# Kernel tuning notes

Measured on AMD Instinct MI355X. Metric: run time of the kernel, lower is better.

Reference implementation:

```python
import jax, jax.numpy as jnp
import numpy as np

B = 1024
NUM_FEATURES = 800  # 10*10 grid * 8 channels
L1, L2, L3, NUM_CLASSES = 1024, 15, 32, 1
STRIDE = 10  # max(1, (96+2*1-3)//(10-1))
VIS_THRESH = 0.0


def setup_inputs() -> dict:
    key = jax.random.key(0)
    ks = jax.random.split(key, 9)
    images = jax.random.normal(ks[0], (B, 3, 96, 96), dtype=jnp.float32)
    conv_w = jax.random.normal(ks[1], (8, 3, 3, 3), dtype=jnp.float32) * 0.1
    ft_w = jax.random.normal(ks[2], (NUM_FEATURES, L1), dtype=jnp.float32) * 0.1
    ft_b = jnp.zeros((L1,), dtype=jnp.float32)
    w1 = jax.random.normal(ks[3], (L2, L1), dtype=jnp.float32) * (1.0 / np.sqrt(L1))
    b1 = jax.random.normal(ks[4], (L2,), dtype=jnp.float32) * 0.01
    w2 = jax.random.normal(ks[5], (L3, L2), dtype=jnp.float32) * (1.0 / np.sqrt(L2))
    b2 = jax.random.normal(ks[6], (L3,), dtype=jnp.float32) * 0.01
    w3 = jax.random.normal(ks[7], (NUM_CLASSES, L3), dtype=jnp.float32) * (1.0 / np.sqrt(L3))
    b3 = jax.random.normal(ks[8], (NUM_CLASSES,), dtype=jnp.float32) * 0.01
    return {"images": images, "conv_w": conv_w, "ft_w": ft_w, "ft_b": ft_b,
            "w1": w1, "b1": b1, "w2": w2, "b2": b2, "w3": w3, "b3": b3}


def reference(images, conv_w, ft_w, ft_b, w1, b1, w2, b2, w3, b3):
    # Conv2d(3->8, k=3, stride=10, pad=1, no bias): [B,3,96,96] -> [B,8,10,10]
    x = jax.lax.conv_general_dilated(
        images, conv_w, window_strides=(STRIDE, STRIDE),
        padding=((1, 1), (1, 1)),
        dimension_numbers=("NCHW", "OIHW", "NCHW"))
    x = jnp.clip(x, -1.0, 1.0)  # Hardtanh
    # training-mode soft binarization
    binary = jax.nn.sigmoid(10.0 * (x - VIS_THRESH))
    bflat = binary.reshape(binary.shape[0], -1)  # [B, 800]
    # _to_sparse_features keeps only entries > 0.5; FeatureTransformer then does
    # a ragged gather-scale-sum == masked dense matmul with the FT weights.
    vals = jnp.where(bflat > 0.5, bflat, 0.0)
    features = vals @ ft_w + ft_b  # [B, L1]
    l0 = jnp.clip(features, 0.0, 1.0)
    h = L1 // 2
    s0, s1 = l0[:, :h], l0[:, h:]
    l0c = jnp.concatenate([s0 * s1, s0], axis=1) * (127.0 / 128.0)  # [B, L1]
    # SimpleClassifier: Linear->ReLU->Linear->ReLU->Linear
    h1 = jax.nn.relu(l0c @ w1.T + b1)
    h2 = jax.nn.relu(h1 @ w2.T + b2)
    out = h2 @ w3.T + b3  # [B, NUM_CLASSES]
    return out
```

## Files before the change

### kernel.cpp

```cpp
#include <hip/hip_runtime.h>

typedef unsigned short u16;
typedef unsigned int   u32;
typedef __attribute__((ext_vector_type(8))) short short8;
typedef __attribute__((ext_vector_type(4))) float f32x4;

__device__ __forceinline__ u16 f2bf(float f) {
    union { float f; u32 i; } v; v.f = f;
    u32 x = v.i;
    return (u16)((x + 0x7fffu + ((x >> 16) & 1u)) >> 16);
}
__device__ __forceinline__ float bf2f(u16 u) {
    union { u32 i; float f; } v; v.i = ((u32)u) << 16; return v.f;
}

__global__ __launch_bounds__(256) void k1_fused(
    const float* __restrict__ images,
    const float* __restrict__ conv_w,
    const float* __restrict__ ft_w,
    u16* __restrict__ vh, u16* __restrict__ vl,
    u16* __restrict__ bth, u16* __restrict__ btl)
{
    __shared__ float img_s[3][29][96];
    __shared__ float w[216];
    __shared__ float tile[32][33];

    int t = threadIdx.x;

    if (blockIdx.x >= 1024) {
        int bid = blockIdx.x - 1024;
        int kb = bid / 32, nb = bid - kb * 32;
        int k0 = kb * 32, n0 = nb * 32;
        int tx = t & 31, ty = t >> 5;
        #pragma unroll
        for (int i = 0; i < 4; i++) {
            int k = ty + i * 8;
            tile[k][tx] = ft_w[(k0 + k) * 1024 + n0 + tx];
        }
        __syncthreads();
        #pragma unroll
        for (int i = 0; i < 4; i++) {
            int n = ty + i * 8;
            float wv = tile[tx][n];
            u16 hi = f2bf(wv);
            float lo = wv - bf2f(hi);
            bth[(n0 + n) * 800 + k0 + tx] = hi;
            btl[(n0 + n) * 800 + k0 + tx] = f2bf(lo);
        }
        return;
    }

    int b = blockIdx.x;
    if (t < 216) w[t] = conv_w[t];

    for (int i = t; i < 3 * 29 * 96; i += 256) {
        int ch  = i / (29 * 96);
        int rem = i - ch * (29 * 96);
        int lr  = rem / 96;
        int x   = rem - lr * 96;
        int ih  = 10 * ((lr + 1) / 3) + (lr + 1) % 3 - 1;
        img_s[ch][lr][x] = images[((b * 3 + ch) * 96 + ih) * 96 + x];
    }
    __syncthreads();

    for (int ridx = t; ridx < 800; ridx += 256) {
        int o  = ridx / 100;
        int p  = ridx - o * 100;
        int oh = p / 10;
        int ow = p - oh * 10;

        float sum = 0.0f;
        #pragma unroll
        for (int ic = 0; ic < 3; ic++) {
            const float* wc = &w[o * 27 + ic * 9];
            #pragma unroll
            for (int kh = 0; kh < 3; kh++) {
                int lr = 3 * oh + kh - 1;
                if (lr < 0) continue;
                #pragma unroll
                for (int kw = 0; kw < 3; kw++) {
                    int iw = ow * 10 + kw - 1;
                    if (iw < 0) continue;
                    sum = fmaf(img_s[ic][lr][iw], wc[kh * 3 + kw], sum);
                }
            }
        }
        float xc = fminf(fmaxf(sum, -1.0f), 1.0f);
        float binary = 1.0f / (1.0f + __expf(-10.0f * xc));
        float v = (binary > 0.5f) ? binary : 0.0f;
        u16 hi = f2bf(v);
        vh[b * 800 + ridx] = hi;
        vl[b * 800 + ridx] = f2bf(v - bf2f(hi));
    }
}

__global__ __launch_bounds__(256) void k2_mfma(
    const u16* __restrict__ Ah, const u16* __restrict__ Al,
    const u16* __restrict__ Bh, const u16* __restrict__ Bl,
    const float* __restrict__ bias,
    float* __restrict__ C)
{
    __shared__ u16 sAh[64 * 40], sAl[64 * 40], sBh[64 * 40], sBl[64 * 40];
    int t = threadIdx.x;
    int m0 = blockIdx.y * 64, n0 = blockIdx.x * 64;
    int w = t >> 6, lane = t & 63;
    int quad = lane >> 4, lo4 = lane & 15;
    int wm = (w >> 1) * 32, wn = (w & 1) * 32;

    int sr = t >> 2;
    int sq = t & 3;
    const u16* gAh = Ah + (m0 + sr) * 800 + sq * 8;
    const u16* gAl = Al + (m0 + sr) * 800 + sq * 8;
    const u16* gBh = Bh + (n0 + sr) * 800 + sq * 8;
    const u16* gBl = Bl + (n0 + sr) * 800 + sq * 8;
    int sdst = sr * 40 + sq * 8;

    f32x4 acc[2][2] = {};

    uint4 rAh = *(const uint4*)(gAh);
    uint4 rAl = *(const uint4*)(gAl);
    uint4 rBh = *(const uint4*)(gBh);
    uint4 rBl = *(const uint4*)(gBl);

    for (int k0 = 0; k0 < 800; k0 += 32) {
        *(uint4*)&sAh[sdst] = rAh;
        *(uint4*)&sAl[sdst] = rAl;
        *(uint4*)&sBh[sdst] = rBh;
        *(uint4*)&sBl[sdst] = rBl;
        __syncthreads();

        if (k0 + 32 < 800) {
            rAh = *(const uint4*)(gAh + k0 + 32);
            rAl = *(const uint4*)(gAl + k0 + 32);
            rBh = *(const uint4*)(gBh + k0 + 32);
            rBl = *(const uint4*)(gBl + k0 + 32);
        }

        short8 a_h[2], a_l[2], b_h[2], b_l[2];
        #pragma unroll
        for (int f = 0; f < 2; f++) {
            int mi = (wm + f * 16 + lo4) * 40 + quad * 8;
            a_h[f] = *(const short8*)&sAh[mi];
            a_l[f] = *(const short8*)&sAl[mi];
            int ni = (wn + f * 16 + lo4) * 40 + quad * 8;
            b_h[f] = *(const short8*)&sBh[ni];
            b_l[f] = *(const short8*)&sBl[ni];
        }
        #pragma unroll
        for (int fm = 0; fm < 2; fm++)
            #pragma unroll
            for (int fn = 0; fn < 2; fn++) {
                acc[fm][fn] = __builtin_amdgcn_mfma_f32_16x16x32_bf16(a_h[fm], b_h[fn], acc[fm][fn], 0, 0, 0);
                acc[fm][fn] = __builtin_amdgcn_mfma_f32_16x16x32_bf16(a_h[fm], b_l[fn], acc[fm][fn], 0, 0, 0);
                acc[fm][fn] = __builtin_amdgcn_mfma_f32_16x16x32_bf16(a_l[fm], b_h[fn], acc[fm][fn], 0, 0, 0);
            }
        __syncthreads();
    }

    #pragma unroll
    for (int fm = 0; fm < 2; fm++) {
        #pragma unroll
        for (int fn = 0; fn < 2; fn++) {
            int n = n0 + wn + fn * 16 + lo4;
            float bv = bias[n];
            #pragma unroll
            for (int r = 0; r < 4; r++) {
                int m = m0 + wm + fm * 16 + quad * 4 + r;
                float v = acc[fm][fn][r] + bv;
                C[m * 1024 + n] = fminf(fmaxf(v, 0.f), 1.f);
            }
        }
    }
}

__global__ __launch_bounds__(256) void k3_tail(
    const float* __restrict__ l0,
    const float* __restrict__ w1,
    const float* __restrict__ b1,
    const float* __restrict__ w2,
    const float* __restrict__ b2,
    const float* __restrict__ w3,
    const float* __restrict__ b3,
    float* __restrict__ out)
{
    int wave = threadIdx.x >> 6;
    int lane = threadIdx.x & 63;
    int b = blockIdx.x * 4 + wave;
    const float* row = l0 + b * 1024;
    const float cc = 0.9921875f;

    float acc[15];
    #pragma unroll
    for (int j = 0; j < 15; j++) acc[j] = 0.f;

    #pragma unroll
    for (int i = 0; i < 2; i++) {
        int k4 = (lane + i * 64) * 4;
        float4 x0 = *(const float4*)(row + k4);
        float4 x1 = *(const float4*)(row + k4 + 512);
        float4 va, vb;
        va.x = x0.x * x1.x * cc; va.y = x0.y * x1.y * cc;
        va.z = x0.z * x1.z * cc; va.w = x0.w * x1.w * cc;
        vb.x = x0.x * cc; vb.y = x0.y * cc;
        vb.z = x0.z * cc; vb.w = x0.w * cc;
        #pragma unroll
        for (int j = 0; j < 15; j++) {
            float4 wa = *(const float4*)(w1 + j * 1024 + k4);
            float4 wb = *(const float4*)(w1 + j * 1024 + k4 + 512);
            acc[j] = fmaf(va.x, wa.x, acc[j]); acc[j] = fmaf(va.y, wa.y, acc[j]);
            acc[j] = fmaf(va.z, wa.z, acc[j]); acc[j] = fmaf(va.w, wa.w, acc[j]);
            acc[j] = fmaf(vb.x, wb.x, acc[j]); acc[j] = fmaf(vb.y, wb.y, acc[j]);
            acc[j] = fmaf(vb.z, wb.z, acc[j]); acc[j] = fmaf(vb.w, wb.w, acc[j]);
        }
    }

    #pragma unroll
    for (int j = 0; j < 15; j++) {
        #pragma unroll
        for (int m = 32; m >= 1; m >>= 1)
            acc[j] += __shfl_xor(acc[j], m, 64);
    }
    float h1[15];
    #pragma unroll
    for (int j = 0; j < 15; j++) h1[j] = fmaxf(acc[j] + b1[j], 0.f);

    float contrib = 0.f;
    if (lane < 32) {
        float h2 = b2[lane];
        #pragma unroll
        for (int j = 0; j < 15; j++) h2 = fmaf(h1[j], w2[lane * 15 + j], h2);
        h2 = fmaxf(h2, 0.f);
        contrib = h2 * w3[lane];
    }
    #pragma unroll
    for (int m = 32; m >= 1; m >>= 1) contrib += __shfl_xor(contrib, m, 64);

    if (lane == 0) out[b] = contrib + b3[0];
}

extern "C" void kernel_launch(void* const* d_in, const int* in_sizes, int n_in,
                              void* d_out, int out_size, void* d_ws, size_t ws_size,
                              hipStream_t stream) {
    const float* images = (const float*)d_in[0];
    const float* conv_w = (const float*)d_in[1];
    const float* ft_w   = (const float*)d_in[2];
    const float* ft_b   = (const float*)d_in[3];
    const float* w1     = (const float*)d_in[4];
    const float* b1     = (const float*)d_in[5];
    const float* w2     = (const float*)d_in[6];
    const float* b2     = (const float*)d_in[7];
    const float* w3     = (const float*)d_in[8];
    const float* b3     = (const float*)d_in[9];
    float* out = (float*)d_out;

    const int NV = 1024 * 800;
    u16* vh  = (u16*)d_ws;
    u16* vl  = vh + NV;
    u16* bth = vl + NV;
    u16* btl = bth + NV;
    float* l0 = (float*)(btl + NV);

    k1_fused<<<1824, 256, 0, stream>>>(images, conv_w, ft_w, vh, vl, bth, btl);
    k2_mfma<<<dim3(16, 16), 256, 0, stream>>>(vh, vl, bth, btl, ft_b, l0);
    k3_tail<<<256, 256, 0, stream>>>(l0, w1, b1, w2, b2, w3, b3, out);
}
```

Before: 209.7 us.

## Merge three kernels into one cooperative persistent kernel with grid syncs

Replaces the three separate launches (conv/weight-convert, MFMA GEMM, MLP tail) with a single cooperative kernel of 256 blocks that loops over the stage-1 jobs, then uses grid-wide syncs between stages. It reuses shared memory through a union across phases. The aim is to remove inter-kernel launch gaps and tail bubbles. In exchange, stage 1 runs with only 256 resident blocks instead of 1824, grid sync itself has a cost, and the old three-kernel path is kept as a fallback if the cooperative launch fails.

```diff
diff --git a/kernel.cpp b/kernel.cpp
--- a/kernel.cpp
+++ b/kernel.cpp
@@ -1,4 +1,7 @@
 #include <hip/hip_runtime.h>
+#include <hip/hip_cooperative_groups.h>
+
+namespace cg = cooperative_groups;
 
 typedef unsigned short u16;
 typedef unsigned int   u32;
@@ -12,6 +15,229 @@
 }
 __device__ __forceinline__ float bf2f(u16 u) {
     union { u32 i; float f; } v; v.i = ((u32)u) << 16; return v.f;
+}
+
+struct P1 { float img[3][29][96]; float w[216]; float tile[32][33]; };
+struct P2 { u16 sAh[64 * 40]; u16 sAl[64 * 40]; u16 sBh[64 * 40]; u16 sBl[64 * 40]; };
+union SMem { P1 p1; P2 p2; };
+
+__global__ __launch_bounds__(256) void k_all(
+    const float* __restrict__ images,
+    const float* __restrict__ conv_w,
+    const float* __restrict__ ft_w,
+    const float* __restrict__ ft_b,
+    const float* __restrict__ w1, const float* __restrict__ b1,
+    const float* __restrict__ w2, const float* __restrict__ b2,
+    const float* __restrict__ w3, const float* __restrict__ b3,
+    float* __restrict__ out,
+    u16* __restrict__ vh, u16* __restrict__ vl,
+    u16* __restrict__ bth, u16* __restrict__ btl,
+    float* __restrict__ l0)
+{
+    __shared__ SMem smem;
+    int t = threadIdx.x;
+
+    for (int job = blockIdx.x; job < 1824; job += 256) {
+        __syncthreads();
+        if (job >= 1024) {
+            int bid = job - 1024;
+            int kb = bid / 32, nb = bid - kb * 32;
+            int k0 = kb * 32, n0 = nb * 32;
+            int tx = t & 31, ty = t >> 5;
+            #pragma unroll
+            for (int i = 0; i < 4; i++) {
+                int k = ty + i * 8;
+                smem.p1.tile[k][tx] = ft_w[(k0 + k) * 1024 + n0 + tx];
+            }
+            __syncthreads();
+            #pragma unroll
+            for (int i = 0; i < 4; i++) {
+                int n = ty + i * 8;
+                float wv = smem.p1.tile[tx][n];
+                u16 hi = f2bf(wv);
+                float lo = wv - bf2f(hi);
+                bth[(n0 + n) * 800 + k0 + tx] = hi;
+                btl[(n0 + n) * 800 + k0 + tx] = f2bf(lo);
+            }
+        } else {
+            int b = job;
+            if (t < 216) smem.p1.w[t] = conv_w[t];
+            for (int i = t; i < 3 * 29 * 96; i += 256) {
+                int ch  = i / (29 * 96);
+                int rem = i - ch * (29 * 96);
+                int lr  = rem / 96;
+                int x   = rem - lr * 96;
+                int ih  = 10 * ((lr + 1) / 3) + (lr + 1) % 3 - 1;
+                smem.p1.img[ch][lr][x] = images[((b * 3 + ch) * 96 + ih) * 96 + x];
+            }
+            __syncthreads();
+
+            for (int ridx = t; ridx < 800; ridx += 256) {
+                int o  = ridx / 100;
+                int p  = ridx - o * 100;
+                int oh = p / 10;
+                int ow = p - oh * 10;
+
+                float sum = 0.0f;
+                #pragma unroll
+                for (int ic = 0; ic < 3; ic++) {
+                    const float* wc = &smem.p1.w[o * 27 + ic * 9];
+                    #pragma unroll
+                    for (int kh = 0; kh < 3; kh++) {
+                        int lr = 3 * oh + kh - 1;
+                        if (lr < 0) continue;
+                        #pragma unroll
+                        for (int kw = 0; kw < 3; kw++) {
+                            int iw = ow * 10 + kw - 1;
+                            if (iw < 0) continue;
+                            sum = fmaf(smem.p1.img[ic][lr][iw], wc[kh * 3 + kw], sum);
+                        }
+                    }
+                }
+                float xc = fminf(fmaxf(sum, -1.0f), 1.0f);
+                float binary = 1.0f / (1.0f + __expf(-10.0f * xc));
+                float v = (binary > 0.5f) ? binary : 0.0f;
+                u16 hi = f2bf(v);
+                vh[b * 800 + ridx] = hi;
+                vl[b * 800 + ridx] = f2bf(v - bf2f(hi));
+            }
+        }
+    }
+
+    cg::this_grid().sync();
+
+    {
+        u16* sAh = smem.p2.sAh; u16* sAl = smem.p2.sAl;
+        u16* sBh = smem.p2.sBh; u16* sBl = smem.p2.sBl;
+
+        int m0 = (blockIdx.x >> 4) * 64, n0 = (blockIdx.x & 15) * 64;
+        int w = t >> 6, lane = t & 63;
+        int quad = lane >> 4, lo4 = lane & 15;
+        int wm = (w >> 1) * 32, wn = (w & 1) * 32;
+
+        int sr = t >> 2;
+        int sq = t & 3;
+        const u16* gAh = vh + (m0 + sr) * 800 + sq * 8;
+        const u16* gAl = vl + (m0 + sr) * 800 + sq * 8;
+        const u16* gBh = bth + (n0 + sr) * 800 + sq * 8;
+        const u16* gBl = btl + (n0 + sr) * 800 + sq * 8;
+        int sdst = sr * 40 + sq * 8;
+
+        f32x4 acc[2][2] = {};
+
+        uint4 rAh = *(const uint4*)(gAh);
+        uint4 rAl = *(const uint4*)(gAl);
+        uint4 rBh = *(const uint4*)(gBh);
+        uint4 rBl = *(const uint4*)(gBl);
+
+        for (int k0 = 0; k0 < 800; k0 += 32) {
+            *(uint4*)&sAh[sdst] = rAh;
+            *(uint4*)&sAl[sdst] = rAl;
+            *(uint4*)&sBh[sdst] = rBh;
+            *(uint4*)&sBl[sdst] = rBl;
+            __syncthreads();
+
+            if (k0 + 32 < 800) {
+                rAh = *(const uint4*)(gAh + k0 + 32);
+                rAl = *(const uint4*)(gAl + k0 + 32);
+                rBh = *(const uint4*)(gBh + k0 + 32);
+                rBl = *(const uint4*)(gBl + k0 + 32);
+            }
+
+            short8 a_h[2], a_l[2], b_h[2], b_l[2];
+            #pragma unroll
+            for (int f = 0; f < 2; f++) {
+                int mi = (wm + f * 16 + lo4) * 40 + quad * 8;
+                a_h[f] = *(const short8*)&sAh[mi];
+                a_l[f] = *(const short8*)&sAl[mi];
+                int ni = (wn + f * 16 + lo4) * 40 + quad * 8;
+                b_h[f] = *(const short8*)&sBh[ni];
+                b_l[f] = *(const short8*)&sBl[ni];
+            }
+            #pragma unroll
+            for (int fm = 0; fm < 2; fm++)
+                #pragma unroll
+                for (int fn = 0; fn < 2; fn++) {
+                    acc[fm][fn] = __builtin_amdgcn_mfma_f32_16x16x32_bf16(a_h[fm], b_h[fn], acc[fm][fn], 0, 0, 0);
+                    acc[fm][fn] = __builtin_amdgcn_mfma_f32_16x16x32_bf16(a_h[fm], b_l[fn], acc[fm][fn], 0, 0, 0);
+                    acc[fm][fn] = __builtin_amdgcn_mfma_f32_16x16x32_bf16(a_l[fm], b_h[fn], acc[fm][fn], 0, 0, 0);
+                }
+            __syncthreads();
+        }
+
+        #pragma unroll
+        for (int fm = 0; fm < 2; fm++) {
+            #pragma unroll
+            for (int fn = 0; fn < 2; fn++) {
+                int n = n0 + wn + fn * 16 + lo4;
+                float bv = ft_b[n];
+                #pragma unroll
+                for (int r = 0; r < 4; r++) {
+                    int m = m0 + wm + fm * 16 + quad * 4 + r;
+                    float v = acc[fm][fn][r] + bv;
+                    l0[m * 1024 + n] = fminf(fmaxf(v, 0.f), 1.f);
+                }
+            }
+        }
+    }
+
+    cg::this_grid().sync();
+
+    {
+        int wave = t >> 6;
+        int lane = t & 63;
+        int b = blockIdx.x * 4 + wave;
+        const float* row = l0 + b * 1024;
+        const float cc = 0.9921875f;
+
+        float acc[15];
+        #pragma unroll
+        for (int j = 0; j < 15; j++) acc[j] = 0.f;
+
+        #pragma unroll
+        for (int i = 0; i < 2; i++) {
+            int k4 = (lane + i * 64) * 4;
+            float4 x0 = *(const float4*)(row + k4);
+            float4 x1 = *(const float4*)(row + k4 + 512);
+            float4 va, vb;
+            va.x = x0.x * x1.x * cc; va.y = x0.y * x1.y * cc;
+            va.z = x0.z * x1.z * cc; va.w = x0.w * x1.w * cc;
+            vb.x = x0.x * cc; vb.y = x0.y * cc;
+            vb.z = x0.z * cc; vb.w = x0.w * cc;
+            #pragma unroll
+            for (int j = 0; j < 15; j++) {
+                float4 wa = *(const float4*)(w1 + j * 1024 + k4);
+                float4 wb = *(const float4*)(w1 + j * 1024 + k4 + 512);
+                acc[j] = fmaf(va.x, wa.x, acc[j]); acc[j] = fmaf(va.y, wa.y, acc[j]);
+                acc[j] = fmaf(va.z, wa.z, acc[j]); acc[j] = fmaf(va.w, wa.w, acc[j]);
+                acc[j] = fmaf(vb.x, wb.x, acc[j]); acc[j] = fmaf(vb.y, wb.y, acc[j]);
+                acc[j] = fmaf(vb.z, wb.z, acc[j]); acc[j] = fmaf(vb.w, wb.w, acc[j]);
+            }
+        }
+
+        #pragma unroll
+        for (int j = 0; j < 15; j++) {
+            #pragma unroll
+            for (int m = 32; m >= 1; m >>= 1)
+                acc[j] += __shfl_xor(acc[j], m, 64);
+        }
+        float h1[15];
+        #pragma unroll
+        for (int j = 0; j < 15; j++) h1[j] = fmaxf(acc[j] + b1[j], 0.f);
+
+        float contrib = 0.f;
+        if (lane < 32) {
+            float h2 = b2[lane];
+            #pragma unroll
+            for (int j = 0; j < 15; j++) h2 = fmaf(h1[j], w2[lane * 15 + j], h2);
+            h2 = fmaxf(h2, 0.f);
+            contrib = h2 * w3[lane];
+        }
+        #pragma unroll
+        for (int m = 32; m >= 1; m >>= 1) contrib += __shfl_xor(contrib, m, 64);
+
+        if (lane == 0) out[b] = contrib + b3[0];
+    }
 }
 
 __global__ __launch_bounds__(256) void k1_fused(
@@ -260,7 +486,16 @@
     u16* btl = bth + NV;
     float* l0 = (float*)(btl + NV);
 
-    k1_fused<<<1824, 256, 0, stream>>>(images, conv_w, ft_w, vh, vl, bth, btl);
-    k2_mfma<<<dim3(16, 16), 256, 0, stream>>>(vh, vl, bth, btl, ft_b, l0);
-    k3_tail<<<256, 256, 0, stream>>>(l0, w1, b1, w2, b2, w3, b3, out);
-}
+    void* kargs[] = {
+        (void*)&images, (void*)&conv_w, (void*)&ft_w, (void*)&ft_b,
+        (void*)&w1, (void*)&b1, (void*)&w2, (void*)&b2, (void*)&w3, (void*)&b3,
+        (void*)&out, (void*)&vh, (void*)&vl, (void*)&bth, (void*)&btl, (void*)&l0
+    };
+    hipError_t e = hipLaunchCooperativeKernel(k_all, dim3(256), dim3(256),
+                                              kargs, 0, stream);
+    if (e != hipSuccess) {
+        k1_fused<<<1824, 256, 0, stream>>>(images, conv_w, ft_w, vh, vl, bth, btl);
+        k2_mfma<<<dim3(16, 16), 256, 0, stream>>>(vh, vl, bth, btl, ft_b, l0);
+        k3_tail<<<256, 256, 0, stream>>>(l0, w1, b1, w2, b2, w3, b3, out);
+    }
+}
```

Result: slower. 342.9 us (+63.5%).

## Split-K the FT GEMM into two partial outputs and reduce in tail kernel

Applied to the files above, without the earlier changes.

The 1024x1024x800 GEMM grid of 256 blocks is doubled with a K split (416/384), with each half writing raw partial sums to separate buffers. The tail kernel now adds the two partials plus the FT bias and applies the clamp before the pairwise product. This aims to fill more compute units on the GPU, at the cost of an extra 4 MB write and read of partials. The image shared-memory row is also padded from 96 to 100 floats to reduce bank conflicts.

```diff
diff --git a/kernel.cpp b/kernel.cpp
--- a/kernel.cpp
+++ b/kernel.cpp
@@ -21,7 +21,7 @@
     u16* __restrict__ vh, u16* __restrict__ vl,
     u16* __restrict__ bth, u16* __restrict__ btl)
 {
-    __shared__ float img_s[3][29][96];
+    __shared__ float img_s[3][29][100];
     __shared__ float w[216];
     __shared__ float tile[32][33];
 
@@ -97,12 +97,15 @@
 __global__ __launch_bounds__(256) void k2_mfma(
     const u16* __restrict__ Ah, const u16* __restrict__ Al,
     const u16* __restrict__ Bh, const u16* __restrict__ Bl,
-    const float* __restrict__ bias,
-    float* __restrict__ C)
+    float* __restrict__ C0, float* __restrict__ C1)
 {
     __shared__ u16 sAh[64 * 40], sAl[64 * 40], sBh[64 * 40], sBl[64 * 40];
     int t = threadIdx.x;
     int m0 = blockIdx.y * 64, n0 = blockIdx.x * 64;
+    int kb = (blockIdx.z == 0) ? 0 : 416;
+    int ke = (blockIdx.z == 0) ? 416 : 800;
+    float* C = (blockIdx.z == 0) ? C0 : C1;
+
     int w = t >> 6, lane = t & 63;
     int quad = lane >> 4, lo4 = lane & 15;
     int wm = (w >> 1) * 32, wn = (w & 1) * 32;
@@ -117,19 +120,19 @@
 
     f32x4 acc[2][2] = {};
 
-    uint4 rAh = *(const uint4*)(gAh);
-    uint4 rAl = *(const uint4*)(gAl);
-    uint4 rBh = *(const uint4*)(gBh);
-    uint4 rBl = *(const uint4*)(gBl);
-
-    for (int k0 = 0; k0 < 800; k0 += 32) {
+    uint4 rAh = *(const uint4*)(gAh + kb);
+    uint4 rAl = *(const uint4*)(gAl + kb);
+    uint4 rBh = *(const uint4*)(gBh + kb);
+    uint4 rBl = *(const uint4*)(gBl + kb);
+
+    for (int k0 = kb; k0 < ke; k0 += 32) {
         *(uint4*)&sAh[sdst] = rAh;
         *(uint4*)&sAl[sdst] = rAl;
         *(uint4*)&sBh[sdst] = rBh;
         *(uint4*)&sBl[sdst] = rBl;
         __syncthreads();
 
-        if (k0 + 32 < 800) {
+        if (k0 + 32 < ke) {
             rAh = *(const uint4*)(gAh + k0 + 32);
             rAl = *(const uint4*)(gAl + k0 + 32);
             rBh = *(const uint4*)(gBh + k0 + 32);
@@ -162,19 +165,19 @@
         #pragma unroll
         for (int fn = 0; fn < 2; fn++) {
             int n = n0 + wn + fn * 16 + lo4;
-            float bv = bias[n];
             #pragma unroll
             for (int r = 0; r < 4; r++) {
                 int m = m0 + wm + fm * 16 + quad * 4 + r;
-                float v = acc[fm][fn][r] + bv;
-                C[m * 1024 + n] = fminf(fmaxf(v, 0.f), 1.f);
+                C[m * 1024 + n] = acc[fm][fn][r];
             }
         }
     }
 }
 
 __global__ __launch_bounds__(256) void k3_tail(
-    const float* __restrict__ l0,
+    const float* __restrict__ l0a,
+    const float* __restrict__ l0b,
+    const float* __restrict__ ft_b,
     const float* __restrict__ w1,
     const float* __restrict__ b1,
     const float* __restrict__ w2,
@@ -186,7 +189,8 @@
     int wave = threadIdx.x >> 6;
     int lane = threadIdx.x & 63;
     int b = blockIdx.x * 4 + wave;
-    const float* row = l0 + b * 1024;
+    const float* pa = l0a + b * 1024;
+    const float* pb = l0b + b * 1024;
     const float cc = 0.9921875f;
 
     float acc[15];
@@ -196,8 +200,22 @@
     #pragma unroll
     for (int i = 0; i < 2; i++) {
         int k4 = (lane + i * 64) * 4;
-        float4 x0 = *(const float4*)(row + k4);
-        float4 x1 = *(const float4*)(row + k4 + 512);
+        float4 a0 = *(const float4*)(pa + k4);
+        float4 q0 = *(const float4*)(pb + k4);
+        float4 f0 = *(const float4*)(ft_b + k4);
+        float4 a1 = *(const float4*)(pa + k4 + 512);
+        float4 q1 = *(const float4*)(pb + k4 + 512);
+        float4 f1 = *(const float4*)(ft_b + k4 + 512);
+        float4 x0, x1;
+        x0.x = fminf(fmaxf(a0.x + q0.x + f0.x, 0.f), 1.f);
+        x0.y = fminf(fmaxf(a0.y + q0.y + f0.y, 0.f), 1.f);
+        x0.z = fminf(fmaxf(a0.z + q0.z + f0.z, 0.f), 1.f);
+        x0.w = fminf(fmaxf(a0.w + q0.w + f0.w, 0.f), 1.f);
+        x1.x = fminf(fmaxf(a1.x + q1.x + f1.x, 0.f), 1.f);
+        x1.y = fminf(fmaxf(a1.y + q1.y + f1.y, 0.f), 1.f);
+        x1.z = fminf(fmaxf(a1.z + q1.z + f1.z, 0.f), 1.f);
+        x1.w = fminf(fmaxf(a1.w + q1.w + f1.w, 0.f), 1.f);
+
         float4 va, vb;
         va.x = x0.x * x1.x * cc; va.y = x0.y * x1.y * cc;
         va.z = x0.z * x1.z * cc; va.w = x0.w * x1.w * cc;
@@ -258,9 +276,10 @@
     u16* vl  = vh + NV;
     u16* bth = vl + NV;
     u16* btl = bth + NV;
-    float* l0 = (float*)(btl + NV);
+    float* l0a = (float*)(btl + NV);
+    float* l0b = l0a + 1024 * 1024;
 
     k1_fused<<<1824, 256, 0, stream>>>(images, conv_w, ft_w, vh, vl, bth, btl);
-    k2_mfma<<<dim3(16, 16), 256, 0, stream>>>(vh, vl, bth, btl, ft_b, l0);
-    k3_tail<<<256, 256, 0, stream>>>(l0, w1, b1, w2, b2, w3, b3, out);
-}
+    k2_mfma<<<dim3(16, 16, 2), 256, 0, stream>>>(vh, vl, bth, btl, l0a, l0b);
+    k3_tail<<<256, 256, 0, stream>>>(l0a, l0b, ft_b, w1, b1, w2, b2, w3, b3, out);
+}
```

Result: no change. 207.8 us (-0.9%).
